# Kernel tuning notes

Hardware: AMD Instinct MI355X
Metric: run time of the kernel (lower is better)

Reference implementation:

```python
import jax, jax.numpy as jnp
import numpy as np

TAU = 0.5      # init kwarg tau
LAMBD = 0.5    # init kwarg lambd
N, D, C = 4096, 1024, 512


def setup_inputs() -> dict:
    key = jax.random.key(0)
    k1, k2, k3 = jax.random.split(key, 3)
    return {
        "layer_embeds": jax.random.normal(k1, (N, D), dtype=jnp.float32),
        "y_true": jax.random.randint(k2, (N,), 0, C),
        "y_pred": jax.random.normal(k3, (N, C), dtype=jnp.float32),
    }


def _clce(x, y_true, y_pred):
    n = x.shape[0]
    # pairwise cosine similarity via one matmul (torch eps = 1e-8)
    norms = jnp.clip(jnp.linalg.norm(x, axis=1, keepdims=True), 1e-8)
    xn = x / norms
    sim = (xn @ xn.T + 1.0) * 0.5 * TAU          # [N, N]

    same = y_true[:, None] == y_true[None, :]    # diagonal is always True
    eye = jnp.eye(n, dtype=bool)
    pos_mask = same & ~eye                        # candidate positives (j != i)
    neg_mask = ~same                              # negatives (excludes diagonal)

    # slot 0: similarity to the FIRST positive j (in j order), else stays 0
    first_pos = jnp.argmax(pos_mask, axis=1)
    has_pos = pos_mask.any(axis=1)
    slot0 = jnp.where(has_pos,
                      jnp.take_along_axis(sim, first_pos[:, None], axis=1)[:, 0],
                      0.0)

    # negatives packed left-to-right into columns 1..; unfilled slots stay 0
    cum = jnp.cumsum(neg_mask, axis=1)            # 1-based slot per negative
    cols = jnp.where(neg_mask, cum, 2 * n - 1)    # non-negatives -> sink col
    rows = jnp.arange(n)[:, None]
    loss_temp = jnp.zeros((n, 2 * n), dtype=sim.dtype)
    loss_temp = loss_temp.at[rows, cols].add(jnp.where(neg_mask, sim, 0.0))
    loss_temp = loss_temp.at[:, 0].set(slot0)
    loss_temp = loss_temp[:, : 2 * n - 1]         # drop sink column -> [N, 2N-1]

    cl = -jax.nn.log_softmax(loss_temp, axis=1)[:, 0]
    cl = cl.sum() / n

    logp = jax.nn.log_softmax(y_pred, axis=1)
    ce = -jnp.take_along_axis(logp, y_true[:, None], axis=1).mean()

    return LAMBD * cl + (1.0 - LAMBD) * ce


def reference(layer_embeds, y_true, y_pred):
    return _clce(layer_embeds, y_true, y_pred)
```

## Files before the change

kernel.cpp:

```cpp
#include <hip/hip_runtime.h>
#include <hip/hip_bf16.h>

#define NR 4096
#define DIM 1024
#define NCLS 512

typedef __attribute__((ext_vector_type(4))) float f32x4;
typedef __attribute__((ext_vector_type(8))) int v8i;

static __device__ __forceinline__ unsigned int q4(float v) {
  unsigned int s = (v < 0.f) ? 8u : 0u;
  float a = fabsf(v);
  unsigned int c;
  if (a < 0.25f) c = 0;
  else if (a < 0.75f) c = 1;
  else if (a < 1.25f) c = 2;
  else if (a < 1.75f) c = 3;
  else if (a < 2.5f) c = 4;
  else if (a < 3.5f) c = 5;
  else if (a < 5.0f) c = 6;
  else c = 7;
  return s | c;
}

__global__ __launch_bounds__(256) void k_prep(const float* __restrict__ x,
                                              const int* __restrict__ y,
                                              const float* __restrict__ yp,
                                              unsigned char* __restrict__ xnp,
                                              int* __restrict__ cnt,
                                              int* __restrict__ fpos,
                                              float* __restrict__ slot0,
                                              float* __restrict__ ce,
                                              float* __restrict__ out) {
  const int b = blockIdx.x;
  const int tid = threadIdx.x;
  if (b < 1024) {
    int row = b * 4 + (tid >> 6);
    int lane = tid & 63;
    const float4* xr = reinterpret_cast<const float4*>(x + (size_t)row * DIM);
    float4 v[4];
    float s = 0.f;
#pragma unroll
    for (int it = 0; it < 4; ++it) {
      v[it] = xr[it * 64 + lane];
      s += v[it].x * v[it].x + v[it].y * v[it].y + v[it].z * v[it].z + v[it].w * v[it].w;
    }
#pragma unroll
    for (int d = 1; d < 64; d <<= 1) s += __shfl_xor(s, d);
    float inv = 32.0f / fmaxf(sqrtf(s), 1e-8f);
    unsigned char* xo = xnp + (size_t)row * 512;
#pragma unroll
    for (int it = 0; it < 4; ++it) {
      int k0 = (it * 64 + lane) * 4;
      int pos = (k0 >> 7) * 64 + ((k0 >> 5) & 3) * 16 + ((k0 & 31) >> 1);
      unsigned int n0 = q4(v[it].x * inv), n1 = q4(v[it].y * inv),
                   n2 = q4(v[it].z * inv), n3 = q4(v[it].w * inv);
      unsigned short pk =
          (unsigned short)(n0 | (n1 << 4) | (n2 << 8) | (n3 << 12));
      *(unsigned short*)(xo + pos) = pk;
    }
  } else if (b < 2048) {
    int row = (b - 1024) * 4 + (tid >> 6);
    int lane = tid & 63;
    const float4* p = reinterpret_cast<const float4*>(yp + (size_t)row * NCLS);
    float4 v0 = p[lane], v1 = p[lane + 64];
    float m = fmaxf(fmaxf(fmaxf(v0.x, v0.y), fmaxf(v0.z, v0.w)),
                    fmaxf(fmaxf(v1.x, v1.y), fmaxf(v1.z, v1.w)));
#pragma unroll
    for (int d = 1; d < 64; d <<= 1) m = fmaxf(m, __shfl_xor(m, d));
    float s = __expf(v0.x - m) + __expf(v0.y - m) + __expf(v0.z - m) + __expf(v0.w - m) +
              __expf(v1.x - m) + __expf(v1.y - m) + __expf(v1.z - m) + __expf(v1.w - m);
#pragma unroll
    for (int d = 1; d < 64; d <<= 1) s += __shfl_xor(s, d);
    if (lane == 0) {
      float py = yp[(size_t)row * NCLS + y[row]];
      ce[row] = logf(s) + m - py;
    }
  } else {
    __shared__ int ys[NR];
    __shared__ int scnt[NCLS], sm1[NCLS], sm2[NCLS];
    for (int j = tid; j < NR; j += 256) ys[j] = y[j];
    for (int c = tid; c < NCLS; c += 256) { scnt[c] = 0; sm1[c] = NR; sm2[c] = NR; }
    __syncthreads();
    for (int i = tid; i < NR; i += 256) {
      int c = ys[i];
      atomicAdd(&scnt[c], 1);
      atomicMin(&sm1[c], i);
    }
    __syncthreads();
    for (int i = tid; i < NR; i += 256) {
      int c = ys[i];
      if (sm1[c] != i) atomicMin(&sm2[c], i);
    }
    __syncthreads();
    for (int i = tid; i < NR; i += 256) {
      int c = ys[i];
      int m1 = sm1[c];
      int j = (m1 == i) ? ((sm2[c] >= NR) ? -1 : sm2[c]) : m1;
      fpos[i] = j;
      slot0[i] = 0.f;
    }
    for (int c = tid; c < NCLS; c += 256) cnt[c] = scnt[c];
    if (tid == 0) out[0] = 0.f;
  }
}


#define STAGE2(SLOT, KT)                                                         \
  {                                                                              \
    const char* _sa = (const char*)xnp +                                         \
        (size_t)(rowbase + srow) * 512 + (size_t)(KT) * 64 + scol;               \
    __builtin_amdgcn_global_load_lds(                                            \
        (const __attribute__((address_space(1))) void*)_sa,                      \
        (__attribute__((address_space(3))) void*)(lds + (SLOT) * 16384 +         \
                                                  tid * 16),                     \
        16, 0, 0);                                                               \
    const char* _sb = (const char*)xnp +                                         \
        (size_t)(colbase + srow) * 512 + (size_t)(KT) * 64 + scol;               \
    __builtin_amdgcn_global_load_lds(                                            \
        (const __attribute__((address_space(1))) void*)_sb,                      \
        (__attribute__((address_space(3))) void*)(lds + (SLOT) * 16384 + 8192 +  \
                                                  tid * 16),                     \
        16, 0, 0);                                                               \
  }

__global__ __launch_bounds__(512, 2) void k_gemm(const unsigned char* __restrict__ xnp,
                                                 const int* __restrict__ y,
                                                 const int* __restrict__ fpos,
                                                 float* __restrict__ part,
                                                 float* __restrict__ slot0) {
  __shared__ char lds[65536];
  const int tid = threadIdx.x;
  const int w = tid >> 6, lane = tid & 63;
  const int wr = w >> 2, wcn = w & 3;
  const int r0 = lane & 15, klo = lane >> 4;

  const int bid = blockIdx.x;
  int t0 = (bid & 7) * 66 + (bid >> 3), rb = 0;
  while (t0 >= 32 - rb) { t0 -= 32 - rb; ++rb; }
  const int cb = rb + t0;
  const int rowbase = rb * 128, colbase = cb * 128;
  const bool offd = (rb != cb);

  const int kread = (klo * 16) ^ ((r0 & 3) << 4);
  const int ABaseW = wr * 4096 + r0 * 64 + kread;
  const int BBaseW = 8192 + wcn * 2048 + r0 * 64 + kread;

  int srow, scol;
  {
    int D = tid * 16;
    int L = D ^ (((D >> 6) & 3) << 4);
    srow = L >> 6;
    scol = L & 63;
  }

  f32x4 acc[4][2] = {};

  STAGE2(0, 0)
  STAGE2(1, 1)
  STAGE2(2, 2)

#pragma unroll
  for (int t = 0; t < 8; ++t) {
    asm volatile("s_waitcnt vmcnt(4)" ::: "memory");
    __builtin_amdgcn_s_barrier();
    {
      const int kt = (t + 3 < 8) ? t + 3 : 7;
      STAGE2((t + 3) & 3, kt)
    }
    const int bufb = (t & 3) * 16384;
    v8i afr[4], bfr[2];
#pragma unroll
    for (int mm = 0; mm < 4; ++mm) {
      int4 t4 = *(const int4*)(lds + bufb + ABaseW + mm * 1024);
      v8i tv = {t4.x, t4.y, t4.z, t4.w, 0, 0, 0, 0};
      afr[mm] = tv;
    }
#pragma unroll
    for (int nf = 0; nf < 2; ++nf) {
      int4 t4 = *(const int4*)(lds + bufb + BBaseW + nf * 1024);
      v8i tv = {t4.x, t4.y, t4.z, t4.w, 0, 0, 0, 0};
      bfr[nf] = tv;
    }
    __builtin_amdgcn_s_setprio(1);
#pragma unroll
    for (int mm = 0; mm < 4; ++mm)
#pragma unroll
      for (int nf = 0; nf < 2; ++nf)
        acc[mm][nf] = __builtin_amdgcn_mfma_scale_f32_16x16x128_f8f6f4(
            afr[mm], bfr[nf], acc[mm][nf], 4, 4,
            0, 0x7F7F7F7F, 0, 0x7F7F7F7F);
    __builtin_amdgcn_s_setprio(0);
  }

  asm volatile("s_waitcnt vmcnt(0)" ::: "memory");
  __syncthreads();

  int* yrow_s = (int*)lds;
  int* ycol_s = (int*)(lds + 512);
  int* frow_s = (int*)(lds + 1024);
  int* fcol_s = (int*)(lds + 1536);
  float* rsum = (float*)(lds + 2048);
  float* csum = (float*)(lds + 4096);
  if (tid < 128) {
    yrow_s[tid] = y[rowbase + tid];
    frow_s[tid] = fpos[rowbase + tid];
  } else if (tid < 256) {
    ycol_s[tid - 128] = y[colbase + tid - 128];
    fcol_s[tid - 128] = fpos[colbase + tid - 128];
  }
  __syncthreads();

  float csn[2] = {0.f, 0.f};
#pragma unroll
  for (int m = 0; m < 4; ++m) {
    float rs[4] = {0.f, 0.f, 0.f, 0.f};
    int rloc[4], yr[4], fr[4];
#pragma unroll
    for (int reg = 0; reg < 4; ++reg) {
      rloc[reg] = wr * 64 + m * 16 + klo * 4 + reg;
      yr[reg] = yrow_s[rloc[reg]];
      fr[reg] = frow_s[rloc[reg]];
    }
#pragma unroll
    for (int nf = 0; nf < 2; ++nf) {
      int cl = wcn * 32 + nf * 16 + r0;
      int yc = ycol_s[cl];
      int fc = fcol_s[cl];
      int gc = colbase + cl;
#pragma unroll
      for (int reg = 0; reg < 4; ++reg) {
        float sv = acc[m][nf][reg] * (1.0f / 4096.f) + 0.25f;
        float e = (yr[reg] == yc) ? 0.f : __expf(sv);
        rs[reg] += e;
        csn[nf] += e;
        int gr = rowbase + rloc[reg];
        if (fr[reg] == gc) slot0[gr] = sv;
        if (offd && fc == gr) slot0[gc] = sv;
      }
    }
#pragma unroll
    for (int d = 1; d < 16; d <<= 1)
#pragma unroll
      for (int reg = 0; reg < 4; ++reg) rs[reg] += __shfl_xor(rs[reg], d);
    if (r0 == 0) {
#pragma unroll
      for (int reg = 0; reg < 4; ++reg)
        rsum[rloc[reg] * 4 + wcn] = rs[reg];
    }
  }
#pragma unroll
  for (int nf = 0; nf < 2; ++nf) {
    csn[nf] += __shfl_xor(csn[nf], 16);
    csn[nf] += __shfl_xor(csn[nf], 32);
  }
  if (klo == 0) {
#pragma unroll
    for (int nf = 0; nf < 2; ++nf)
      csum[(wcn * 32 + nf * 16 + r0) * 2 + wr] = csn[nf];
  }
  __syncthreads();
  if (tid < 128) {
    part[(size_t)cb * NR + rowbase + tid] =
        rsum[tid * 4] + rsum[tid * 4 + 1] + rsum[tid * 4 + 2] + rsum[tid * 4 + 3];
    if (offd)
      part[(size_t)rb * NR + colbase + tid] = csum[tid * 2] + csum[tid * 2 + 1];
  }
}

__global__ __launch_bounds__(256) void k_final(const float* __restrict__ part,
                                               const float* __restrict__ slot0,
                                               const int* __restrict__ cnt,
                                               const int* __restrict__ y,
                                               const float* __restrict__ ce,
                                               float* __restrict__ out) {
  __shared__ float red[256];
  const int tid = threadIdx.x;
  const int r = blockIdx.x * 256 + tid;
  float S = 0.f;
#pragma unroll
  for (int b = 0; b < 32; ++b) S += part[(size_t)b * NR + r];
  float s0 = slot0[r];
  float zeros = 4094.0f + (float)cnt[y[r]];
  float cl = logf(__expf(s0) + S + zeros) - s0;
  red[tid] = 0.5f * (cl + ce[r]);
  __syncthreads();
  for (int s = 128; s > 0; s >>= 1) {
    if (tid < s) red[tid] += red[tid + s];
    __syncthreads();
  }
  if (tid == 0) atomicAdd(out, red[0] / (float)NR);
}

extern "C" void kernel_launch(void* const* d_in, const int* in_sizes, int n_in,
                              void* d_out, int out_size, void* d_ws, size_t ws_size,
                              hipStream_t stream) {
  const float* x = (const float*)d_in[0];
  const int* y = (const int*)d_in[1];
  const float* yp = (const float*)d_in[2];
  float* out = (float*)d_out;

  char* w = (char*)d_ws;
  unsigned char* xnp = (unsigned char*)w;
  int* cnt = (int*)(w + 2097152);
  int* fpos = (int*)(w + 2099200);
  float* slot0 = (float*)(w + 2115584);
  float* part = (float*)(w + 2131968);
  float* ce = (float*)(w + 2656256);

  k_prep<<<2049, 256, 0, stream>>>(x, y, yp, xnp, cnt, fpos, slot0, ce, out);
  k_gemm<<<528, 512, 0, stream>>>(xnp, y, fpos, part, slot0);
  k_final<<<16, 256, 0, stream>>>(part, slot0, cnt, y, ce, out);
}
```

Before: 45.45 us.

## Load GEMM fragments directly from global memory instead of LDS staging

Drops the four-slot LDS ring buffer, which was filled with global_load_lds and gated by waitcnt and barriers. Each wave now reads its FP4 A and B fragments straight from global memory into registers and relies on L1/L2 for reuse across waves. The LDS allocation shrinks to the epilogue scratch space, and the barriers and setprio hints in the K loop go away. In exchange, each wave issues redundant global loads and loses explicit prefetch. Latency hiding now depends on the compiler hoisting loads in the fully unrolled 8-step loop.

```diff
diff --git a/kernel.cpp b/kernel.cpp
--- a/kernel.cpp
+++ b/kernel.cpp
@@ -106,30 +106,12 @@
 }
 
 
-#define STAGE2(SLOT, KT)                                                         \
-  {                                                                              \
-    const char* _sa = (const char*)xnp +                                         \
-        (size_t)(rowbase + srow) * 512 + (size_t)(KT) * 64 + scol;               \
-    __builtin_amdgcn_global_load_lds(                                            \
-        (const __attribute__((address_space(1))) void*)_sa,                      \
-        (__attribute__((address_space(3))) void*)(lds + (SLOT) * 16384 +         \
-                                                  tid * 16),                     \
-        16, 0, 0);                                                               \
-    const char* _sb = (const char*)xnp +                                         \
-        (size_t)(colbase + srow) * 512 + (size_t)(KT) * 64 + scol;               \
-    __builtin_amdgcn_global_load_lds(                                            \
-        (const __attribute__((address_space(1))) void*)_sb,                      \
-        (__attribute__((address_space(3))) void*)(lds + (SLOT) * 16384 + 8192 +  \
-                                                  tid * 16),                     \
-        16, 0, 0);                                                               \
-  }
-
 __global__ __launch_bounds__(512, 2) void k_gemm(const unsigned char* __restrict__ xnp,
                                                  const int* __restrict__ y,
                                                  const int* __restrict__ fpos,
                                                  float* __restrict__ part,
                                                  float* __restrict__ slot0) {
-  __shared__ char lds[65536];
+  __shared__ char lds[8192];
   const int tid = threadIdx.x;
   const int w = tid >> 6, lane = tid & 63;
   const int wr = w >> 2, wcn = w & 3;
@@ -142,47 +124,28 @@
   const int rowbase = rb * 128, colbase = cb * 128;
   const bool offd = (rb != cb);
 
-  const int kread = (klo * 16) ^ ((r0 & 3) << 4);
-  const int ABaseW = wr * 4096 + r0 * 64 + kread;
-  const int BBaseW = 8192 + wcn * 2048 + r0 * 64 + kread;
-
-  int srow, scol;
-  {
-    int D = tid * 16;
-    int L = D ^ (((D >> 6) & 3) << 4);
-    srow = L >> 6;
-    scol = L & 63;
-  }
+  const unsigned char* abase =
+      xnp + (size_t)(rowbase + wr * 64 + r0) * 512 + klo * 16;
+  const unsigned char* bbase =
+      xnp + (size_t)(colbase + wcn * 32 + r0) * 512 + klo * 16;
 
   f32x4 acc[4][2] = {};
 
-  STAGE2(0, 0)
-  STAGE2(1, 1)
-  STAGE2(2, 2)
-
 #pragma unroll
   for (int t = 0; t < 8; ++t) {
-    asm volatile("s_waitcnt vmcnt(4)" ::: "memory");
-    __builtin_amdgcn_s_barrier();
-    {
-      const int kt = (t + 3 < 8) ? t + 3 : 7;
-      STAGE2((t + 3) & 3, kt)
-    }
-    const int bufb = (t & 3) * 16384;
     v8i afr[4], bfr[2];
 #pragma unroll
     for (int mm = 0; mm < 4; ++mm) {
-      int4 t4 = *(const int4*)(lds + bufb + ABaseW + mm * 1024);
+      int4 t4 = *(const int4*)(abase + mm * 8192 + t * 64);
       v8i tv = {t4.x, t4.y, t4.z, t4.w, 0, 0, 0, 0};
       afr[mm] = tv;
     }
 #pragma unroll
     for (int nf = 0; nf < 2; ++nf) {
-      int4 t4 = *(const int4*)(lds + bufb + BBaseW + nf * 1024);
+      int4 t4 = *(const int4*)(bbase + nf * 8192 + t * 64);
       v8i tv = {t4.x, t4.y, t4.z, t4.w, 0, 0, 0, 0};
       bfr[nf] = tv;
     }
-    __builtin_amdgcn_s_setprio(1);
 #pragma unroll
     for (int mm = 0; mm < 4; ++mm)
 #pragma unroll
@@ -190,11 +153,7 @@
         acc[mm][nf] = __builtin_amdgcn_mfma_scale_f32_16x16x128_f8f6f4(
             afr[mm], bfr[nf], acc[mm][nf], 4, 4,
             0, 0x7F7F7F7F, 0, 0x7F7F7F7F);
-    __builtin_amdgcn_s_setprio(0);
-  }
-
-  asm volatile("s_waitcnt vmcnt(0)" ::: "memory");
-  __syncthreads();
+  }
 
   int* yrow_s = (int*)lds;
   int* ycol_s = (int*)(lds + 512);
```

Result: slower. 66.53 us (+46.4%).
